# Optimization experiments

Measured on AMD Instinct MI355X. Metric: run time of the kernel, lower is better.

Reference implementation:

```python
import jax, jax.numpy as jnp
import numpy as np

# Single LSTM cell step from ZERO initial state (h0=c0=0), vectorized over (B,T).
# PyTorch gate order: i, f, g, o. Since h0=0 the W_hh contribution is exactly 0
# and since c0=0 the forget-gate term vanishes: c = sigmoid(i)*tanh(g).

def _cell(inp, W_ih, b_ih, b_hh):
    # inp: (B,T,in), W_ih: (4H,in) -> gates (B,T,4H)
    g = jnp.einsum('bti,gi->btg', inp, W_ih) + b_ih + b_hh
    i_, f_, g_, o_ = jnp.split(g, 4, axis=-1)
    c = jax.nn.sigmoid(i_) * jnp.tanh(g_)
    h = jax.nn.sigmoid(o_) * jnp.tanh(c)
    return h, c


def setup_inputs() -> dict:
    key = jax.random.key(0)
    ks = jax.random.split(key, 11)
    B, T, E, H, V = 32, 256, 512, 512, 50000
    s = 1.0 / np.sqrt(H)  # keep gates out of deep saturation
    return {
        'x': jax.random.randint(ks[0], (B, T), 0, V, dtype=jnp.int32),
        'emb': jax.random.normal(ks[1], (V, E), jnp.float32),
        'W_ih_l0': jax.random.normal(ks[2], (2, 4 * H, E), jnp.float32) * s,
        'W_hh_l0': jax.random.normal(ks[3], (2, 4 * H, H), jnp.float32) * s,
        'b_ih_l0': jax.random.normal(ks[4], (2, 4 * H), jnp.float32) * s,
        'b_hh_l0': jax.random.normal(ks[5], (2, 4 * H), jnp.float32) * s,
        'W_ih_l1': jax.random.normal(ks[6], (2, 4 * H, 2 * H), jnp.float32) * s,
        'W_hh_l1': jax.random.normal(ks[7], (2, 4 * H, H), jnp.float32) * s,
        'b_ih_l1': jax.random.normal(ks[8], (2, 4 * H), jnp.float32) * s,
        'b_hh_l1': jax.random.normal(ks[9], (2, 4 * H), jnp.float32) * s,
    }


def reference(x, emb, W_ih_l0, W_hh_l0, b_ih_l0, b_hh_l0,
              W_ih_l1, W_hh_l1, b_ih_l1, b_hh_l1):
    e = emb[x]  # (B,T,E)
    # layer 0, forward/backward directions (seq_len==1 per step, so both
    # directions see the same token from zero state, with separate weights)
    h0f, c0f = _cell(e, W_ih_l0[0], b_ih_l0[0], b_hh_l0[0])
    h0b, c0b = _cell(e, W_ih_l0[1], b_ih_l0[1], b_hh_l0[1])
    inp1 = jnp.concatenate([h0f, h0b], axis=-1)  # (B,T,2H)
    h1f, c1f = _cell(inp1, W_ih_l1[0], b_ih_l1[0], b_hh_l1[0])
    h1b, c1b = _cell(inp1, W_ih_l1[1], b_ih_l1[1], b_hh_l1[1])
    # encoder_out: per-timestep h_n summed over directions -> (B,T,L,H)
    encoder_out = jnp.stack([h0f + h0b, h1f + h1b], axis=2)
    # h_last: forward-direction h_n and c_n at last timestep -> (L,B,H)
    h_last = jnp.stack([h0f[:, -1], h1f[:, -1]], axis=0)
    c_last = jnp.stack([c0f[:, -1], c1f[:, -1]], axis=0)
    return h_last, c_last, encoder_out
```

## Files before the change

kernel.cpp:

```cpp
#include <hip/hip_runtime.h>
#include <hip/hip_bf16.h>


using bf16x8 = __attribute__((ext_vector_type(8))) short;
using f32x4  = __attribute__((ext_vector_type(4))) float;

__device__ __forceinline__ unsigned short f2bf(float f)
{
    __hip_bfloat16 h = __float2bfloat16(f);
    return *(unsigned short*)&h;
}
__device__ __forceinline__ float sigf(float x)  { return 1.0f / (1.0f + __expf(-x)); }
__device__ __forceinline__ float tanhfast(float x)
{
    return 1.0f - 2.0f / (__expf(2.0f * x) + 1.0f);
}

__device__ __forceinline__ void gload16(const void* g, void* l)
{
    __builtin_amdgcn_global_load_lds(
        (const __attribute__((address_space(1))) unsigned int*)g,
        (__attribute__((address_space(3))) unsigned int*)l, 16, 0, 0);
}
#define SBAR() do { __builtin_amdgcn_sched_barrier(0); \
                    __builtin_amdgcn_s_barrier();      \
                    __builtin_amdgcn_sched_barrier(0); } while (0)

__global__ __launch_bounds__(256)
void prep(const int* __restrict__ x, const void* __restrict__ emb,
          const void* __restrict__ Wih0, const void* __restrict__ Wih1,
          const void* __restrict__ bih0, const void* __restrict__ bhh0,
          const void* __restrict__ bih1, const void* __restrict__ bhh1,
          uint4* __restrict__ e0, uint4* __restrict__ Wp0, uint4* __restrict__ Wp1,
          float* __restrict__ bc0, float* __restrict__ bc1, int* __restrict__ flag)
{
    __shared__ int oks[4];
    {
        unsigned lo = ((const unsigned int*)emb)[threadIdx.x] & 0xFFFFu;
        int e = (lo >> 7) & 0xFF;
        int ok = ((e >= 96 && e < 160) || lo == 0) ? 1 : 0;
#pragma unroll
        for (int off = 32; off; off >>= 1) ok += __shfl_down(ok, off);
        if ((threadIdx.x & 63) == 0) oks[threadIdx.x >> 6] = ok;
    }
    __syncthreads();
    const bool isbf = (oks[0] + oks[1] + oks[2] + oks[3]) >= 192;
    const int bid = blockIdx.x, tid = threadIdx.x;

    if (bid < 2048) {
        int idx = bid * 256 + tid;
        int k8 = idx >> 13, m = idx & 8191;
        long srow = x[m];
        uint4 v;
        if (isbf) {
            v = ((const uint4*)emb)[srow * 64 + k8];
        } else {
            const float4* ef = (const float4*)emb;
            float4 a = ef[srow * 128 + k8 * 2], b = ef[srow * 128 + k8 * 2 + 1];
            unsigned short h[8] = { f2bf(a.x), f2bf(a.y), f2bf(a.z), f2bf(a.w),
                                    f2bf(b.x), f2bf(b.y), f2bf(b.z), f2bf(b.w) };
            v = *(uint4*)h;
        }
        e0[idx] = v;
    } else if (bid < 4352) {
        const bool L0 = bid < 2816;
        int idx = (L0 ? (bid - 2048) : (bid - 2816)) * 256 + tid;
        int k8 = idx / 3072, n = idx - k8 * 3072;
        int h = n / 6, gi = n - h * 6;
        int dir = (gi >= 3) ? 1 : 0;
        int gate = gi - dir * 3;
        int sg = (gate == 0) ? 0 : (gate + 1);
        long srcrow = dir * 2048 + sg * 512 + h;
        const void* src = L0 ? Wih0 : Wih1;
        uint4* dst = L0 ? Wp0 : Wp1;
        const int K4 = L0 ? 128 : 256, K8 = L0 ? 64 : 128;
        if (isbf) {
            dst[idx] = ((const uint4*)src)[srcrow * K8 + k8];
        } else {
            const float4* sf = (const float4*)src;
            float4 a = sf[srcrow * K4 + k8 * 2], b = sf[srcrow * K4 + k8 * 2 + 1];
            unsigned short h8[8] = { f2bf(a.x), f2bf(a.y), f2bf(a.z), f2bf(a.w),
                                     f2bf(b.x), f2bf(b.y), f2bf(b.z), f2bf(b.w) };
            dst[idx] = *(uint4*)h8;
        }
    } else {
        int b2 = bid - 4352;
        if (b2 == 0 && tid == 0) *flag = isbf ? 1 : 0;
        const bool L0 = b2 < 12;
        int n = (L0 ? b2 : (b2 - 12)) * 256 + tid;
        int h = n / 6, gi = n - h * 6;
        int dir = (gi >= 3) ? 1 : 0;
        int gate = gi - dir * 3;
        int sg = (gate == 0) ? 0 : (gate + 1);
        int s = dir * 2048 + sg * 512 + h;
        const void* bi = L0 ? bih0 : bih1;
        const void* bh = L0 ? bhh0 : bhh1;
        float* bc = L0 ? bc0 : bc1;
        float vi, vh;
        if (isbf) {
            vi = __bfloat162float(((const __hip_bfloat16*)bi)[s]);
            vh = __bfloat162float(((const __hip_bfloat16*)bh)[s]);
        } else {
            vi = ((const float*)bi)[s];
            vh = ((const float*)bh)[s];
        }
        bc[n] = vi + vh;
    }
}

template <int LAYER>
__global__ __launch_bounds__(512)
void gemm_fused(const unsigned short* __restrict__ A,
                const unsigned short* __restrict__ Bp,
                const float* __restrict__ bc,
                unsigned short* __restrict__ inp1,
                void* __restrict__ outv,
                const int* __restrict__ flag,
                int K)
{
    __shared__ __align__(16) char smem[45072];

    const int tid = threadIdx.x;
    const int raw = blockIdx.x + (blockIdx.y << 5);
    const int xcd = raw & 7, local = raw >> 3;
    const int bm = xcd * 4 + (local >> 5);
    const int bn = local & 31;

    const uint4* a4 = (const uint4*)A;
    const uint4* b4 = (const uint4*)Bp;

    const int aRow = bm * 256 + (tid & 255);
    const int aK   = tid >> 8;
    const int bK   = (tid < 384) ? (tid / 96) : 0;
    const int bN   = bn * 96 + ((tid < 384) ? (tid - (tid / 96) * 96) : 0);
    const bool bact = tid < 384;

    const int wave = tid >> 6, lane = tid & 63;
    const int wr = (wave >> 1) * 64;
    const int wc = (wave & 1) * 48;
    const int lr = lane & 15, q = lane >> 4;

    f32x4 acc[4][3] = {};
    const int NT = K >> 5;

    auto stage = [&](int t) {
        const int buf = t & 1;
        const int k8b = t * 4;
        uint4* As4 = (uint4*)(smem + buf * 16384);
        uint4* Bs4 = (uint4*)(smem + 32768 + buf * 6144);
        const uint4* s0 = a4 + (long)(k8b + aK) * 8192 + aRow;
        gload16(s0, As4 + tid);
        gload16(s0 + 2L * 8192, As4 + tid + 512);
        if (bact) gload16(b4 + (long)(k8b + bK) * 3072 + bN, Bs4 + tid);
        else      gload16(s0, (uint4*)(smem + 45056));
    };

    stage(0);
    for (int t = 0; t < NT; ++t) {
        if (t + 1 < NT) {
            stage(t + 1);
            asm volatile("s_waitcnt vmcnt(3)" ::: "memory");
        } else {
            asm volatile("s_waitcnt vmcnt(0)" ::: "memory");
        }
        SBAR();

        const unsigned short* As = (const unsigned short*)(smem + (t & 1) * 16384);
        const unsigned short* Bs = (const unsigned short*)(smem + 32768 + (t & 1) * 6144);
        bf16x8 af[4], bf[3];
#pragma unroll
        for (int i = 0; i < 4; ++i)
            af[i] = *(const bf16x8*)&As[(q * 256 + wr + i * 16 + lr) * 8];
#pragma unroll
        for (int j = 0; j < 3; ++j)
            bf[j] = *(const bf16x8*)&Bs[(q * 96 + wc + j * 16 + lr) * 8];
        __builtin_amdgcn_s_setprio(1);
#pragma unroll
        for (int i = 0; i < 4; ++i)
#pragma unroll
            for (int j = 0; j < 3; ++j)
                acc[i][j] = __builtin_amdgcn_mfma_f32_16x16x32_bf16(af[i], bf[j], acc[i][j], 0, 0, 0);
        __builtin_amdgcn_s_setprio(0);
        SBAR();
    }

    float* Cs = (float*)smem;
    const bool isbf = (*flag != 0);
    auto store = [&](long i, float v) {
        if (isbf) ((__hip_bfloat16*)outv)[i] = __float2bfloat16(v);
        else      ((float*)outv)[i] = v;
    };

    const int hl = tid & 15;
    float bcv[6];
#pragma unroll
    for (int gi = 0; gi < 6; ++gi) bcv[gi] = bc[bn * 96 + hl * 6 + gi];

    for (int p = 0; p < 4; ++p) {
        if ((wave >> 1) == p) {
#pragma unroll
            for (int i = 0; i < 4; ++i)
#pragma unroll
                for (int j = 0; j < 3; ++j)
#pragma unroll
                    for (int r = 0; r < 4; ++r)
                        Cs[(i * 16 + q * 4 + r) * 97 + wc + j * 16 + lr] = acc[i][j][r];
        }
        __syncthreads();
#pragma unroll
        for (int t2 = 0; t2 < 2; ++t2) {
            int ml = (tid >> 4) + t2 * 32;
            float z[6];
#pragma unroll
            for (int gi = 0; gi < 6; ++gi) z[gi] = Cs[ml * 97 + hl * 6 + gi] + bcv[gi];
            float c0 = sigf(z[0]) * tanhfast(z[1]);
            float h0 = sigf(z[2]) * tanhfast(c0);
            float c1 = sigf(z[3]) * tanhfast(z[4]);
            float h1 = sigf(z[5]) * tanhfast(c1);

            long m = (long)bm * 256 + p * 64 + ml;
            int hg = bn * 16 + hl;

            if constexpr (LAYER == 0) {
                int c0i = hg, c1i = 512 + hg;
                inp1[((long)(c0i >> 3) * 8192 + m) * 8 + (c0i & 7)] = f2bf(h0);
                inp1[((long)(c1i >> 3) * 8192 + m) * 8 + (c1i & 7)] = f2bf(h1);
            }
            store(65536 + m * 1024 + LAYER * 512 + hg, h0 + h1);
            if ((m & 255) == 255) {
                int b = (int)(m >> 8);
                store(LAYER * 16384 + b * 512 + hg, h0);
                store(32768 + LAYER * 16384 + b * 512 + hg, c0);
            }
        }
        if (p < 3) __syncthreads();
    }
}

extern "C" void kernel_launch(void* const* d_in, const int* in_sizes, int n_in,
                              void* d_out, int out_size, void* d_ws, size_t ws_size,
                              hipStream_t stream)
{
    const int* x      = (const int*)d_in[0];
    const void* emb   = d_in[1];
    const void* Wih0  = d_in[2];
    const void* bih0  = d_in[4];
    const void* bhh0  = d_in[5];
    const void* Wih1  = d_in[6];
    const void* bih1  = d_in[8];
    const void* bhh1  = d_in[9];

    char* ws = (char*)d_ws;
    int*   flag           = (int*)(ws);
    float* bc0            = (float*)(ws + 1024);
    float* bc1            = (float*)(ws + 16384);
    unsigned short* Wp0   = (unsigned short*)(ws + 32768);
    unsigned short* Wp1   = (unsigned short*)(ws + 4194304);
    unsigned short* e0    = (unsigned short*)(ws + 10485760);
    unsigned short* inp1  = (unsigned short*)(ws + 18874368);

    prep<<<4376, 256, 0, stream>>>(x, emb, Wih0, Wih1, bih0, bhh0, bih1, bhh1,
                                   (uint4*)e0, (uint4*)Wp0, (uint4*)Wp1, bc0, bc1, flag);

    gemm_fused<0><<<dim3(32, 32), 512, 0, stream>>>(e0, Wp0, bc0, inp1, d_out, flag, 512);
    gemm_fused<1><<<dim3(32, 32), 512, 0, stream>>>(inp1, Wp1, bc1, nullptr, d_out, flag, 1024);
}
```

Baseline: 295.1 us.

## Triple-buffer GEMM K pipeline and tile-transpose prep gathers through LDS

The GEMM kernels move from double to triple buffering with two stages in flight and adjusted vmcnt waits. K becomes a template parameter so the K loop can be fully unrolled. The prep kernel now has each block gather a 32-row panel into LDS and write it out transposed, which makes both the reads and the K-major writes coalesced, and the grid shrinks from 4376 to 568 blocks. The cost is more LDS per GEMM block, which may reduce occupancy, plus a sync in prep.

```diff
diff --git a/kernel.cpp b/kernel.cpp
--- a/kernel.cpp
+++ b/kernel.cpp
@@ -35,6 +35,7 @@
           float* __restrict__ bc0, float* __restrict__ bc1, int* __restrict__ flag)
 {
     __shared__ int oks[4];
+    __shared__ uint4 panel[32][65];
     {
         unsigned lo = ((const unsigned int*)emb)[threadIdx.x] & 0xFFFFu;
         int e = (lo >> 7) & 0xFF;
@@ -47,44 +48,72 @@
     const bool isbf = (oks[0] + oks[1] + oks[2] + oks[3]) >= 192;
     const int bid = blockIdx.x, tid = threadIdx.x;
 
-    if (bid < 2048) {
-        int idx = bid * 256 + tid;
-        int k8 = idx >> 13, m = idx & 8191;
-        long srow = x[m];
-        uint4 v;
-        if (isbf) {
-            v = ((const uint4*)emb)[srow * 64 + k8];
-        } else {
-            const float4* ef = (const float4*)emb;
-            float4 a = ef[srow * 128 + k8 * 2], b = ef[srow * 128 + k8 * 2 + 1];
-            unsigned short h[8] = { f2bf(a.x), f2bf(a.y), f2bf(a.z), f2bf(a.w),
-                                    f2bf(b.x), f2bf(b.y), f2bf(b.z), f2bf(b.w) };
-            v = *(uint4*)h;
-        }
-        e0[idx] = v;
-    } else if (bid < 4352) {
-        const bool L0 = bid < 2816;
-        int idx = (L0 ? (bid - 2048) : (bid - 2816)) * 256 + tid;
-        int k8 = idx / 3072, n = idx - k8 * 3072;
-        int h = n / 6, gi = n - h * 6;
-        int dir = (gi >= 3) ? 1 : 0;
-        int gate = gi - dir * 3;
-        int sg = (gate == 0) ? 0 : (gate + 1);
-        long srcrow = dir * 2048 + sg * 512 + h;
+    if (bid < 256) {
+        const int mbase = bid * 32;
+#pragma unroll
+        for (int j = 0; j < 8; ++j) {
+            int li = j * 256 + tid;
+            int ml = li >> 6, k8 = li & 63;
+            long srow = x[mbase + ml];
+            uint4 v;
+            if (isbf) {
+                v = ((const uint4*)emb)[srow * 64 + k8];
+            } else {
+                const float4* ef = (const float4*)emb;
+                float4 a = ef[srow * 128 + k8 * 2], b = ef[srow * 128 + k8 * 2 + 1];
+                unsigned short h[8] = { f2bf(a.x), f2bf(a.y), f2bf(a.z), f2bf(a.w),
+                                        f2bf(b.x), f2bf(b.y), f2bf(b.z), f2bf(b.w) };
+                v = *(uint4*)h;
+            }
+            panel[ml][k8] = v;
+        }
+        __syncthreads();
+#pragma unroll
+        for (int j = 0; j < 8; ++j) {
+            int li = j * 256 + tid;
+            int k8 = li >> 5, ml = li & 31;
+            e0[(long)k8 * 8192 + mbase + ml] = panel[ml][k8];
+        }
+    } else if (bid < 544) {
+        const bool L0 = bid < 352;
+        const int t = L0 ? (bid - 256) : (bid - 352);
+        const int nbase  = (L0 ? t : (t >> 1)) * 32;
+        const int k8base = L0 ? 0 : (t & 1) * 64;
         const void* src = L0 ? Wih0 : Wih1;
         uint4* dst = L0 ? Wp0 : Wp1;
-        const int K4 = L0 ? 128 : 256, K8 = L0 ? 64 : 128;
-        if (isbf) {
-            dst[idx] = ((const uint4*)src)[srcrow * K8 + k8];
-        } else {
-            const float4* sf = (const float4*)src;
-            float4 a = sf[srcrow * K4 + k8 * 2], b = sf[srcrow * K4 + k8 * 2 + 1];
-            unsigned short h8[8] = { f2bf(a.x), f2bf(a.y), f2bf(a.z), f2bf(a.w),
-                                     f2bf(b.x), f2bf(b.y), f2bf(b.z), f2bf(b.w) };
-            dst[idx] = *(uint4*)h8;
+        const int K8s = L0 ? 64 : 128;
+#pragma unroll
+        for (int j = 0; j < 8; ++j) {
+            int li = j * 256 + tid;
+            int nl = li >> 6, k8l = li & 63;
+            int n = nbase + nl;
+            int h = n / 6, gi = n - h * 6;
+            int dir = (gi >= 3) ? 1 : 0;
+            int gate = gi - dir * 3;
+            int sg = (gate == 0) ? 0 : (gate + 1);
+            long srcrow = dir * 2048 + sg * 512 + h;
+            uint4 v;
+            if (isbf) {
+                v = ((const uint4*)src)[srcrow * K8s + k8base + k8l];
+            } else {
+                const float4* sf = (const float4*)src;
+                long c2 = (srcrow * K8s + k8base + k8l) * 2;
+                float4 a = sf[c2], b = sf[c2 + 1];
+                unsigned short h8[8] = { f2bf(a.x), f2bf(a.y), f2bf(a.z), f2bf(a.w),
+                                         f2bf(b.x), f2bf(b.y), f2bf(b.z), f2bf(b.w) };
+                v = *(uint4*)h8;
+            }
+            panel[nl][k8l] = v;
+        }
+        __syncthreads();
+#pragma unroll
+        for (int j = 0; j < 8; ++j) {
+            int li = j * 256 + tid;
+            int k8l = li >> 5, nl = li & 31;
+            dst[(long)(k8base + k8l) * 3072 + nbase + nl] = panel[nl][k8l];
         }
     } else {
-        int b2 = bid - 4352;
+        int b2 = bid - 544;
         if (b2 == 0 && tid == 0) *flag = isbf ? 1 : 0;
         const bool L0 = b2 < 12;
         int n = (L0 ? b2 : (b2 - 12)) * 256 + tid;
@@ -108,17 +137,17 @@
     }
 }
 
-template <int LAYER>
+template <int LAYER, int K>
 __global__ __launch_bounds__(512)
 void gemm_fused(const unsigned short* __restrict__ A,
                 const unsigned short* __restrict__ Bp,
                 const float* __restrict__ bc,
                 unsigned short* __restrict__ inp1,
                 void* __restrict__ outv,
-                const int* __restrict__ flag,
-                int K)
-{
-    __shared__ __align__(16) char smem[45072];
+                const int* __restrict__ flag)
+{
+    constexpr int NT = K / 32;
+    __shared__ __align__(16) char smem[67584];
 
     const int tid = threadIdx.x;
     const int raw = blockIdx.x + (blockIdx.y << 5);
@@ -129,11 +158,9 @@
     const uint4* a4 = (const uint4*)A;
     const uint4* b4 = (const uint4*)Bp;
 
-    const int aRow = bm * 256 + (tid & 255);
-    const int aK   = tid >> 8;
-    const int bK   = (tid < 384) ? (tid / 96) : 0;
-    const int bN   = bn * 96 + ((tid < 384) ? (tid - (tid / 96) * 96) : 0);
-    const bool bact = tid < 384;
+    const int btid = (tid < 384) ? tid : (tid - 128);
+    const long aOff = (long)(tid >> 8) * 8192 + bm * 256 + (tid & 255);
+    const long bOff = (long)(btid / 96) * 3072 + bn * 96 + (btid % 96);
 
     const int wave = tid >> 6, lane = tid & 63;
     const int wr = (wave >> 1) * 64;
@@ -141,32 +168,33 @@
     const int lr = lane & 15, q = lane >> 4;
 
     f32x4 acc[4][3] = {};
-    const int NT = K >> 5;
-
-    auto stage = [&](int t) {
-        const int buf = t & 1;
-        const int k8b = t * 4;
+
+    auto stage = [&](int s) {
+        const int buf = s % 3;
         uint4* As4 = (uint4*)(smem + buf * 16384);
-        uint4* Bs4 = (uint4*)(smem + 32768 + buf * 6144);
-        const uint4* s0 = a4 + (long)(k8b + aK) * 8192 + aRow;
-        gload16(s0, As4 + tid);
-        gload16(s0 + 2L * 8192, As4 + tid + 512);
-        if (bact) gload16(b4 + (long)(k8b + bK) * 3072 + bN, Bs4 + tid);
-        else      gload16(s0, (uint4*)(smem + 45056));
+        uint4* Bs4 = (uint4*)(smem + 49152 + buf * 6144);
+        const uint4* ap = a4 + (long)s * 32768 + aOff;
+        gload16(ap, As4 + tid);
+        gload16(ap + 16384, As4 + tid + 512);
+        gload16(b4 + (long)s * 12288 + bOff, Bs4 + btid);
     };
 
     stage(0);
+    stage(1);
+#pragma unroll
     for (int t = 0; t < NT; ++t) {
-        if (t + 1 < NT) {
-            stage(t + 1);
+        if (t + 2 < NT) {
+            stage(t + 2);
+            asm volatile("s_waitcnt vmcnt(6)" ::: "memory");
+        } else if (t + 1 < NT) {
             asm volatile("s_waitcnt vmcnt(3)" ::: "memory");
         } else {
             asm volatile("s_waitcnt vmcnt(0)" ::: "memory");
         }
         SBAR();
 
-        const unsigned short* As = (const unsigned short*)(smem + (t & 1) * 16384);
-        const unsigned short* Bs = (const unsigned short*)(smem + 32768 + (t & 1) * 6144);
+        const unsigned short* As = (const unsigned short*)(smem + (t % 3) * 16384);
+        const unsigned short* Bs = (const unsigned short*)(smem + 49152 + (t % 3) * 6144);
         bf16x8 af[4], bf[3];
 #pragma unroll
         for (int i = 0; i < 4; ++i)
@@ -259,9 +287,9 @@
     unsigned short* e0    = (unsigned short*)(ws + 10485760);
     unsigned short* inp1  = (unsigned short*)(ws + 18874368);
 
-    prep<<<4376, 256, 0, stream>>>(x, emb, Wih0, Wih1, bih0, bhh0, bih1, bhh1,
-                                   (uint4*)e0, (uint4*)Wp0, (uint4*)Wp1, bc0, bc1, flag);
-
-    gemm_fused<0><<<dim3(32, 32), 512, 0, stream>>>(e0, Wp0, bc0, inp1, d_out, flag, 512);
-    gemm_fused<1><<<dim3(32, 32), 512, 0, stream>>>(inp1, Wp1, bc1, nullptr, d_out, flag, 1024);
-}
+    prep<<<568, 256, 0, stream>>>(x, emb, Wih0, Wih1, bih0, bhh0, bih1, bhh1,
+                                  (uint4*)e0, (uint4*)Wp0, (uint4*)Wp1, bc0, bc1, flag);
+
+    gemm_fused<0, 512><<<dim3(32, 32), 512, 0, stream>>>(e0, Wp0, bc0, inp1, d_out, flag);
+    gemm_fused<1, 1024><<<dim3(32, 32), 512, 0, stream>>>(inp1, Wp1, bc1, nullptr, d_out, flag);
+}
```

New measurement: 287.6 us. 2.5% less time.
